# Kernel optimization log

Measured on AMD Instinct MI355X. Metric: run time of the kernel, lower is better.

## Reference

```python
import jax, jax.numpy as jnp
import numpy as np

FEATURE_DIM = 768
NUM_HEADS = 16
HEAD_DIM = FEATURE_DIM // NUM_HEADS
SCALE = HEAD_DIM ** -0.5


def setup_inputs() -> dict:
    key = jax.random.key(0)
    ks = jax.random.split(key, 9)
    B, N, C = 4, 2048, FEATURE_DIM
    s = 0.02
    return {
        "x": jax.random.normal(ks[0], (B, N, C), dtype=jnp.float32),
        "wq": jax.random.normal(ks[1], (C, C), dtype=jnp.float32) * s,
        "bq": jax.random.normal(ks[2], (C,), dtype=jnp.float32) * s,
        "wk": jax.random.normal(ks[3], (C, C), dtype=jnp.float32) * s,
        "bk": jax.random.normal(ks[4], (C,), dtype=jnp.float32) * s,
        "wv": jax.random.normal(ks[5], (C, C), dtype=jnp.float32) * s,
        "bv": jax.random.normal(ks[6], (C,), dtype=jnp.float32) * s,
        "wo": jax.random.normal(ks[7], (C, C), dtype=jnp.float32) * s,
        "bo": jax.random.normal(ks[8], (C,), dtype=jnp.float32) * s,
    }


def reference(x, wq, bq, wk, bk, wv, bv, wo, bo):
    B, N, C = x.shape
    H, D = NUM_HEADS, HEAD_DIM
    # Linear layers use weight of shape (out, in): y = x @ W.T + b
    def proj(w, b):
        return (jnp.einsum("bnc,dc->bnd", x, w) + b).reshape(B, N, H, D).transpose(0, 2, 1, 3)
    q = proj(wq, bq)  # [B,H,N,D]
    k = proj(wk, bk)
    v = proj(wv, bv)
    attn = jnp.einsum("bhnd,bhmd->bhnm", q, k) * SCALE
    attn = jax.nn.softmax(attn, axis=-1)  # dropout = identity (eval mode)
    y = jnp.einsum("bhnm,bhmd->bhnd", attn, v).transpose(0, 2, 1, 3).reshape(B, N, C)
    y = y + x
    out = jnp.einsum("bnc,dc->bnd", y, wo) + bo
    out = out + y
    return out + x
```

## Files before the change

kernel.cpp:

```cpp
#include <hip/hip_runtime.h>
#include <hip/hip_bf16.h>

#define B_ 4
#define N_ 2048
#define C_ 768
#define H_ 16
#define D_ 48
#define SCALE_ 0.14433756729740643f
#define LOG2E_ 1.44269504088896f

using bf16 = __hip_bfloat16;
using bf16x8 = __attribute__((ext_vector_type(8))) short;
using f32x4  = __attribute__((ext_vector_type(4))) float;
using f32x16 = __attribute__((ext_vector_type(16))) float;
using u32x2  = __attribute__((ext_vector_type(2))) unsigned int;
using u32x4  = __attribute__((ext_vector_type(4))) unsigned int;

__device__ __forceinline__ unsigned short f2b(float f) {
  bf16 h = __float2bfloat16(f);
  return *reinterpret_cast<unsigned short*>(&h);
}
__device__ __forceinline__ unsigned int pack2(float lo, float hi) {
  return (unsigned int)f2b(lo) | ((unsigned int)f2b(hi) << 16);
}
__device__ __forceinline__ unsigned int pk2(float lo, float hi) {
  unsigned int r;
  asm("v_cvt_pk_bf16_f32 %0, %1, %2" : "=v"(r) : "v"(lo), "v"(hi));
  return r;
}
__device__ __forceinline__ uint4 ld8f_cvt(const float* p) {
  float4 a = *reinterpret_cast<const float4*>(p);
  float4 b = *reinterpret_cast<const float4*>(p + 4);
  uint4 u;
  u.x = pack2(a.x, a.y); u.y = pack2(a.z, a.w);
  u.z = pack2(b.x, b.y); u.w = pack2(b.z, b.w);
  return u;
}
__device__ __forceinline__ void gload_lds16(const bf16* g, bf16* l) {
  __builtin_amdgcn_global_load_lds(
      (const __attribute__((address_space(1))) unsigned int*)g,
      (__attribute__((address_space(3))) unsigned int*)l, 16, 0, 0);
}

__global__ __launch_bounds__(256) void cvt_bf16(
    const float* __restrict__ x,  const float* __restrict__ wq,
    const float* __restrict__ wk, const float* __restrict__ wv,
    const float* __restrict__ wo,
    bf16* __restrict__ xb, bf16* __restrict__ wqkvb, bf16* __restrict__ wob)
{
  const int job = blockIdx.y;
  const float* src; bf16* dst; int n;
  if (job == 0)      { src = x;  dst = xb;              n = B_ * N_ * C_; }
  else if (job == 1) { src = wq; dst = wqkvb;           n = C_ * C_; }
  else if (job == 2) { src = wk; dst = wqkvb + C_ * C_; n = C_ * C_; }
  else if (job == 3) { src = wv; dst = wqkvb + 2 * C_ * C_; n = C_ * C_; }
  else               { src = wo; dst = wob;             n = C_ * C_; }
  const int stride = gridDim.x * 256 * 8;
  for (int i = (blockIdx.x * 256 + threadIdx.x) * 8; i < n; i += stride)
    *(uint4*)(dst + i) = ld8f_cvt(src + i);
}

__global__ __launch_bounds__(256) void gemm_qkv(
    const bf16* __restrict__ A, const bf16* __restrict__ Bw,
    const float* __restrict__ bq, const float* __restrict__ bk,
    const float* __restrict__ bv,
    bf16* __restrict__ Q, bf16* __restrict__ K, bf16* __restrict__ V)
{
  __shared__ __align__(16) bf16 As[128 * 64];
  __shared__ __align__(16) bf16 Bs[128 * 64];

  const int tid  = threadIdx.x;
  const int lane = tid & 63, wid = tid >> 6;
  const int wm = (wid >> 1) * 64, wn = (wid & 1) * 64;
  const int row0 = blockIdx.y * 128, col0 = blockIdx.x * 128;
  const int mb = lane & 15, g4 = lane >> 4;
  const int srow = lane >> 3;
  const int schunk = (lane & 7) ^ (srow & 7);

  f32x4 acc[4][4];
#pragma unroll
  for (int i = 0; i < 4; ++i)
#pragma unroll
    for (int j = 0; j < 4; ++j) acc[i][j] = (f32x4){0.f, 0.f, 0.f, 0.f};

  for (int k0 = 0; k0 < C_; k0 += 64) {
#pragma unroll
    for (int t = 0; t < 4; ++t) {
      const int rt = wid * 32 + t * 8;
      gload_lds16(A  + (size_t)(row0 + rt + srow) * C_ + k0 + schunk * 8,
                  As + rt * 64);
      gload_lds16(Bw + (size_t)(col0 + rt + srow) * C_ + k0 + schunk * 8,
                  Bs + rt * 64);
    }
    __syncthreads();
#pragma unroll
    for (int ks = 0; ks < 2; ++ks) {
      const int kchunk = ks * 4 + g4;
      bf16x8 af[4], bfr[4];
#pragma unroll
      for (int i = 0; i < 4; ++i) {
        const int row = wm + i * 16 + mb;
        af[i] = *(const bf16x8*)(As + row * 64 + (kchunk ^ (row & 7)) * 8);
      }
#pragma unroll
      for (int j = 0; j < 4; ++j) {
        const int col = wn + j * 16 + mb;
        bfr[j] = *(const bf16x8*)(Bs + col * 64 + (kchunk ^ (col & 7)) * 8);
      }
#pragma unroll
      for (int i = 0; i < 4; ++i)
#pragma unroll
        for (int j = 0; j < 4; ++j)
          acc[i][j] = __builtin_amdgcn_mfma_f32_16x16x32_bf16(af[i], bfr[j], acc[i][j], 0, 0, 0);
    }
    __syncthreads();
  }

  const int z = blockIdx.x / 6;
  const float* bias = (z == 0) ? bq : (z == 1) ? bk : bv;
  bf16* dst = (z == 0) ? Q : (z == 1) ? K : V;
  const float sc = (z == 0) ? (SCALE_ * LOG2E_) : 1.0f;
  const int crow = g4 * 4;
#pragma unroll
  for (int j = 0; j < 4; ++j) {
    const int oo = col0 - z * 768 + wn + j * 16 + mb;
    const int h = oo / D_, d = oo % D_;
    const float bb = bias[oo];
#pragma unroll
    for (int i = 0; i < 4; ++i) {
#pragma unroll
      for (int reg = 0; reg < 4; ++reg) {
        const int r = row0 + wm + i * 16 + crow + reg;
        const int b_ = r >> 11, n = r & (N_ - 1);
        dst[(((size_t)(b_ * H_ + h)) * N_ + n) * D_ + d] =
            __float2bfloat16((acc[i][j][reg] + bb) * sc);
      }
    }
  }
}

__global__ __launch_bounds__(256) void qkv_reshape(
    bf16* __restrict__ Q, bf16* __restrict__ K,
    const bf16* __restrict__ Vtmp, bf16* __restrict__ Vf)
{
  __shared__ short T[64 * 50];
  const int bh = blockIdx.x;
  const int t0 = blockIdx.y * 64;
  const int tid = threadIdx.x;
  const size_t base = (size_t)bh * (N_ * D_) + (size_t)t0 * D_;
#pragma unroll 1
  for (int wbuf = 0; wbuf < 2; ++wbuf) {
    bf16* P = (wbuf ? K : Q) + base;
    for (int cc = tid; cc < 384; cc += 256) {
      const int r = cc / 6, ch = cc % 6;
      bf16x8 v8 = *(const bf16x8*)(P + r * D_ + ch * 8);
#pragma unroll
      for (int e = 0; e < 8; ++e) T[r * 50 + ch * 8 + e] = v8[e];
    }
    __syncthreads();
    for (int w = tid; w < 384; w += 256) {
      const int sub = w / 192, rem = w % 192;
      const int kc = rem / 64, rem2 = rem % 64;
      const int g2 = rem2 >> 5, m5 = rem2 & 31;
      bf16x8 o;
#pragma unroll
      for (int e = 0; e < 8; ++e)
        o[e] = T[(sub * 32 + m5) * 50 + kc * 16 + g2 * 8 + e];
      *(bf16x8*)(P + w * 8) = o;
    }
    __syncthreads();
  }
  {
    const bf16* Pv = Vtmp + base;
    for (int cc = tid; cc < 384; cc += 256) {
      const int r = cc / 6, ch = cc % 6;
      bf16x8 v8 = *(const bf16x8*)(Pv + r * D_ + ch * 8);
#pragma unroll
      for (int e = 0; e < 8; ++e) T[r * 50 + ch * 8 + e] = v8[e];
    }
    __syncthreads();
    bf16* W = Vf + (size_t)bh * (N_ * 64) + (size_t)t0 * 64;
    for (int w = tid; w < 512; w += 256) {
      const int ksl = w >> 7;
      const int dt  = (w >> 6) & 1;
      const int l   = w & 63;
      const int hi = l >> 5, m5 = l & 31;
      bf16x8 o;
      if (dt == 0) {
#pragma unroll
        for (int e = 0; e < 8; ++e)
          o[e] = T[(ksl * 16 + hi * 8 + e) * 50 + m5];
      } else if (m5 < 16) {
#pragma unroll
        for (int e = 0; e < 8; ++e)
          o[e] = T[(ksl * 16 + hi * 8 + e) * 50 + 32 + m5];
      } else {
        const short fill = (m5 == 16) ? (short)0x3F80 : (short)0;
#pragma unroll
        for (int e = 0; e < 8; ++e) o[e] = fill;
      }
      *(bf16x8*)(W + (size_t)(((ksl * 2 + dt) * 64 + l) * 8)) = o;
    }
  }
}

__global__ __launch_bounds__(256, 4) void attn_mfma(
    const bf16* __restrict__ Qf, const bf16* __restrict__ Kf,
    const bf16* __restrict__ Vf, const float* __restrict__ x,
    bf16* __restrict__ Yb)
{
  __shared__ __align__(16) bf16 Ls[2 * 7168];

  const int tid  = threadIdx.x;
  const int lane = tid & 63, wid = tid >> 6;
  const int m5 = lane & 31, hi = lane >> 5;
  const int bh = blockIdx.x;
  const int b_ = bh >> 4, h = bh & 15;
  const int q0 = blockIdx.y * 128 + wid * 32;
  const size_t slab  = (size_t)bh * (N_ * D_);
  const size_t slabV = (size_t)bh * (N_ * 64);

  bf16x8 qf[3];
  const int kgq = q0 >> 5;
#pragma unroll
  for (int kc = 0; kc < 3; ++kc)
    qf[kc] = *(const bf16x8*)(Qf + slab + (size_t)(((kgq * 3 + kc) * 64) + lane) * 8);

  f32x16 zf;
#pragma unroll
  for (int r = 0; r < 16; ++r) zf[r] = 0.f;

  f32x16 Oacc[2];
#pragma unroll
  for (int dt = 0; dt < 2; ++dt)
#pragma unroll
    for (int r = 0; r < 16; ++r) Oacc[dt][r] = 0.f;

  const bf16* kb = Kf + slab  + (size_t)lane * 8;
  const bf16* vb = Vf + slabV + (size_t)lane * 8;
  auto stage = [&](int t, int buf) {
    bf16* dstb = Ls + buf * 7168;
    const bf16* kt = kb + (size_t)t * 3072;
    const bf16* vt = vb + (size_t)t * 4096;
    for (int c = wid; c < 14; c += 4) {
      if (c < 6) gload_lds16(kt + c * 512, dstb + c * 512);
      else       gload_lds16(vt + (c - 6) * 512, dstb + c * 512);
    }
  };

  auto sub = [&](int buf, int s) {
    const bf16* Lb = Ls + buf * 7168 + (size_t)lane * 8;
    bf16x8 kf[3], vA[2][2];
#pragma unroll
    for (int kc = 0; kc < 3; ++kc)
      kf[kc] = *(const bf16x8*)(Lb + (s * 3 + kc) * 512);
#pragma unroll
    for (int ks = 0; ks < 2; ++ks)
#pragma unroll
      for (int dt = 0; dt < 2; ++dt)
        vA[ks][dt] = *(const bf16x8*)(Lb + (6 + s * 4 + ks * 2 + dt) * 512);
    f32x16 S;
    S = __builtin_amdgcn_mfma_f32_32x32x16_bf16(kf[0], qf[0], zf, 0, 0, 0);
    S = __builtin_amdgcn_mfma_f32_32x32x16_bf16(kf[1], qf[1], S, 0, 0, 0);
    S = __builtin_amdgcn_mfma_f32_32x32x16_bf16(kf[2], qf[2], S, 0, 0, 0);
#pragma unroll
    for (int r = 0; r < 16; ++r)
      S[r] = __builtin_amdgcn_exp2f(S[r]);
#pragma unroll
    for (int ks = 0; ks < 2; ++ks) {
      const int qa = ks * 2;
      const unsigned A0 = pk2(S[4 * qa + 0], S[4 * qa + 1]);
      const unsigned A1 = pk2(S[4 * qa + 2], S[4 * qa + 3]);
      const unsigned B0 = pk2(S[4 * qa + 4], S[4 * qa + 5]);
      const unsigned B1 = pk2(S[4 * qa + 6], S[4 * qa + 7]);
      const u32x2 r02 = __builtin_amdgcn_permlane32_swap(A0, B0, false, false);
      const u32x2 r13 = __builtin_amdgcn_permlane32_swap(A1, B1, false, false);
      u32x4 pw;
      pw.x = r02.x; pw.y = r13.x; pw.z = r02.y; pw.w = r13.y;
      const bf16x8 pb = (bf16x8)pw;
      Oacc[0] = __builtin_amdgcn_mfma_f32_32x32x16_bf16(vA[ks][0], pb, Oacc[0], 0, 0, 0);
      Oacc[1] = __builtin_amdgcn_mfma_f32_32x32x16_bf16(vA[ks][1], pb, Oacc[1], 0, 0, 0);
    }
  };

  stage(0, 0);
  __syncthreads();
  int buf = 0;
#pragma unroll 1
  for (int t = 0; t < 32; ++t) {
    if (t + 1 < 32) stage(t + 1, buf ^ 1);
    sub(buf, 0);
    sub(buf, 1);
    __syncthreads();
    buf ^= 1;
  }

  const float lf = Oacc[1][8];
  const unsigned lu = __builtin_bit_cast(unsigned, lf);
  const u32x2 lsw = __builtin_amdgcn_permlane32_swap(lu, lu, false, false);
  const float Lv = __builtin_bit_cast(float, lsw.x);
  const float inv = 1.f / Lv;

  const int n = q0 + m5;
  const size_t rowoff = ((size_t)(b_ * N_ + n)) * C_ + h * D_;
#pragma unroll
  for (int qq = 0; qq < 4; ++qq) {
    const size_t off = rowoff + 8 * qq + 4 * hi;
    const float4 xr = *(const float4*)(x + off);
    u32x2 wv;
    wv.x = pk2(Oacc[0][4 * qq + 0] * inv + xr.x, Oacc[0][4 * qq + 1] * inv + xr.y);
    wv.y = pk2(Oacc[0][4 * qq + 2] * inv + xr.z, Oacc[0][4 * qq + 3] * inv + xr.w);
    *(u32x2*)(Yb + off) = wv;
  }
#pragma unroll
  for (int qq = 0; qq < 2; ++qq) {
    const size_t off = rowoff + 32 + 8 * qq + 4 * hi;
    const float4 xr = *(const float4*)(x + off);
    u32x2 wv;
    wv.x = pk2(Oacc[1][4 * qq + 0] * inv + xr.x, Oacc[1][4 * qq + 1] * inv + xr.y);
    wv.y = pk2(Oacc[1][4 * qq + 2] * inv + xr.z, Oacc[1][4 * qq + 3] * inv + xr.w);
    *(u32x2*)(Yb + off) = wv;
  }
}

__global__ __launch_bounds__(256) void gemm_out(
    const bf16* __restrict__ Yb, const bf16* __restrict__ Bw,
    const float* __restrict__ bo, const float* __restrict__ x,
    float* __restrict__ out)
{
  __shared__ __align__(16) bf16 As[128 * 64];
  __shared__ __align__(16) bf16 Bs[128 * 64];

  const int tid  = threadIdx.x;
  const int lane = tid & 63, wid = tid >> 6;
  const int wm = (wid >> 1) * 64, wn = (wid & 1) * 64;
  const int row0 = blockIdx.y * 128, col0 = blockIdx.x * 128;
  const int mb = lane & 15, g4 = lane >> 4;
  const int srow = lane >> 3;
  const int schunk = (lane & 7) ^ (srow & 7);

  f32x4 acc[4][4];
#pragma unroll
  for (int i = 0; i < 4; ++i)
#pragma unroll
    for (int j = 0; j < 4; ++j) acc[i][j] = (f32x4){0.f, 0.f, 0.f, 0.f};

  for (int k0 = 0; k0 < C_; k0 += 64) {
#pragma unroll
    for (int t = 0; t < 4; ++t) {
      const int rt = wid * 32 + t * 8;
      gload_lds16(Yb + (size_t)(row0 + rt + srow) * C_ + k0 + schunk * 8,
                  As + rt * 64);
      gload_lds16(Bw + (size_t)(col0 + rt + srow) * C_ + k0 + schunk * 8,
                  Bs + rt * 64);
    }
    __syncthreads();
#pragma unroll
    for (int ks = 0; ks < 2; ++ks) {
      const int kchunk = ks * 4 + g4;
      bf16x8 af[4], bfr[4];
#pragma unroll
      for (int i = 0; i < 4; ++i) {
        const int row = wm + i * 16 + mb;
        af[i] = *(const bf16x8*)(As + row * 64 + (kchunk ^ (row & 7)) * 8);
      }
#pragma unroll
      for (int j = 0; j < 4; ++j) {
        const int col = wn + j * 16 + mb;
        bfr[j] = *(const bf16x8*)(Bs + col * 64 + (kchunk ^ (col & 7)) * 8);
      }
#pragma unroll
      for (int i = 0; i < 4; ++i)
#pragma unroll
        for (int j = 0; j < 4; ++j)
          acc[i][j] = __builtin_amdgcn_mfma_f32_16x16x32_bf16(af[i], bfr[j], acc[i][j], 0, 0, 0);
    }
    __syncthreads();
  }

  const int crow = g4 * 4;
#pragma unroll
  for (int j = 0; j < 4; ++j) {
    const int o = col0 + wn + j * 16 + mb;
    const float bb = bo[o];
#pragma unroll
    for (int i = 0; i < 4; ++i) {
#pragma unroll
      for (int reg = 0; reg < 4; ++reg) {
        const int r = row0 + wm + i * 16 + crow + reg;
        const size_t off = (size_t)r * C_ + o;
        out[off] = acc[i][j][reg] + bb + __bfloat162float(Yb[off]) + x[off];
      }
    }
  }
}

extern "C" void kernel_launch(void* const* d_in, const int* in_sizes, int n_in,
                              void* d_out, int out_size, void* d_ws, size_t ws_size,
                              hipStream_t stream)
{
  const float* x  = (const float*)d_in[0];
  const float* wq = (const float*)d_in[1];
  const float* bq = (const float*)d_in[2];
  const float* wk = (const float*)d_in[3];
  const float* bk = (const float*)d_in[4];
  const float* wv = (const float*)d_in[5];
  const float* bv = (const float*)d_in[6];
  const float* wo = (const float*)d_in[7];
  const float* bo = (const float*)d_in[8];
  float* out = (float*)d_out;

  const size_t nEl  = (size_t)B_ * N_ * C_;
  const size_t wEl  = (size_t)C_ * C_;
  const size_t vfEl = (size_t)B_ * H_ * N_ * 64;
  bf16* Q     = (bf16*)d_ws;
  bf16* K     = Q + nEl;
  bf16* Vf    = K + nEl;
  bf16* Yb    = Vf + vfEl;
  bf16* xb    = Yb + nEl;
  bf16* wqkvb = xb + nEl;
  bf16* wob   = wqkvb + 3 * wEl;

  dim3 gcvt(768, 5);
  cvt_bf16<<<gcvt, dim3(256), 0, stream>>>(x, wq, wk, wv, wo, xb, wqkvb, wob);

  dim3 gqkv(18, 64);
  gemm_qkv<<<gqkv, dim3(256), 0, stream>>>(xb, wqkvb, bq, bk, bv, Q, K, Yb);

  dim3 grs(B_ * H_, N_ / 64);
  qkv_reshape<<<grs, dim3(256), 0, stream>>>(Q, K, Yb, Vf);

  dim3 gattn(B_ * H_, N_ / 128);
  attn_mfma<<<gattn, dim3(256), 0, stream>>>(Q, K, Vf, x, Yb);

  dim3 gout(6, 64);
  gemm_out<<<gout, dim3(256), 0, stream>>>(Yb, wob, bo, x, out);
}
```

Baseline: 261.7 us.

## Fuse QKV reshape into GEMM epilogue and triple-buffer attention K/V staging

The QKV GEMM epilogue now writes Q, K and V straight into the MFMA-ready tiled layouts the attention kernel reads, which removes the separate reshape kernel and its extra global round trip. The constant padding columns of the V layout are filled by an extra job in the conversion kernel. Separately, the attention kernel moves to a three-deep LDS ring with only two waves issuing loads, uses explicit vmcnt waits plus a raw barrier in place of syncthreads, and raises wave priority around MFMA bursts. These changes add LDS usage and make correctness depend on the hand-written waitcnt accounting.

Measured after the change: 262.0 us. No clear change (+0.1%).

```diff
diff --git a/kernel.cpp b/kernel.cpp
--- a/kernel.cpp
+++ b/kernel.cpp
@@ -46,9 +46,22 @@
     const float* __restrict__ x,  const float* __restrict__ wq,
     const float* __restrict__ wk, const float* __restrict__ wv,
     const float* __restrict__ wo,
-    bf16* __restrict__ xb, bf16* __restrict__ wqkvb, bf16* __restrict__ wob)
+    bf16* __restrict__ xb, bf16* __restrict__ wqkvb, bf16* __restrict__ wob,
+    bf16* __restrict__ vfp)
 {
   const int job = blockIdx.y;
+  if (job == 5) {
+    for (int u = blockIdx.x * 256 + threadIdx.x; u < 64 * 128 * 32;
+         u += gridDim.x * 256) {
+      const int m5i = u & 15, hb = (u >> 4) & 1, n4 = (u >> 5) & 127,
+                bh = u >> 12;
+      const short fill = (m5i == 0) ? (short)0x3F80 : (short)0;
+      const bf16x8 o = {fill, fill, fill, fill, fill, fill, fill, fill};
+      *(bf16x8*)(vfp + (size_t)bh * 131072 + n4 * 1024 + 512 + hb * 256 +
+                 (16 + m5i) * 8) = o;
+    }
+    return;
+  }
   const float* src; bf16* dst; int n;
   if (job == 0)      { src = x;  dst = xb;              n = B_ * N_ * C_; }
   else if (job == 1) { src = wq; dst = wqkvb;           n = C_ * C_; }
@@ -64,7 +77,7 @@
     const bf16* __restrict__ A, const bf16* __restrict__ Bw,
     const float* __restrict__ bq, const float* __restrict__ bk,
     const float* __restrict__ bv,
-    bf16* __restrict__ Q, bf16* __restrict__ K, bf16* __restrict__ V)
+    bf16* __restrict__ Q, bf16* __restrict__ K, bf16* __restrict__ Vf)
 {
   __shared__ __align__(16) bf16 As[128 * 64];
   __shared__ __align__(16) bf16 Bs[128 * 64];
@@ -117,89 +130,45 @@
   }
 
   const int z = blockIdx.x / 6;
-  const float* bias = (z == 0) ? bq : (z == 1) ? bk : bv;
-  bf16* dst = (z == 0) ? Q : (z == 1) ? K : V;
-  const float sc = (z == 0) ? (SCALE_ * LOG2E_) : 1.0f;
-  const int crow = g4 * 4;
-#pragma unroll
-  for (int j = 0; j < 4; ++j) {
-    const int oo = col0 - z * 768 + wn + j * 16 + mb;
-    const int h = oo / D_, d = oo % D_;
-    const float bb = bias[oo];
-#pragma unroll
-    for (int i = 0; i < 4; ++i) {
-#pragma unroll
-      for (int reg = 0; reg < 4; ++reg) {
-        const int r = row0 + wm + i * 16 + crow + reg;
-        const int b_ = r >> 11, n = r & (N_ - 1);
-        dst[(((size_t)(b_ * H_ + h)) * N_ + n) * D_ + d] =
-            __float2bfloat16((acc[i][j][reg] + bb) * sc);
-      }
-    }
-  }
-}
-
-__global__ __launch_bounds__(256) void qkv_reshape(
-    bf16* __restrict__ Q, bf16* __restrict__ K,
-    const bf16* __restrict__ Vtmp, bf16* __restrict__ Vf)
-{
-  __shared__ short T[64 * 50];
-  const int bh = blockIdx.x;
-  const int t0 = blockIdx.y * 64;
-  const int tid = threadIdx.x;
-  const size_t base = (size_t)bh * (N_ * D_) + (size_t)t0 * D_;
-#pragma unroll 1
-  for (int wbuf = 0; wbuf < 2; ++wbuf) {
-    bf16* P = (wbuf ? K : Q) + base;
-    for (int cc = tid; cc < 384; cc += 256) {
-      const int r = cc / 6, ch = cc % 6;
-      bf16x8 v8 = *(const bf16x8*)(P + r * D_ + ch * 8);
-#pragma unroll
-      for (int e = 0; e < 8; ++e) T[r * 50 + ch * 8 + e] = v8[e];
-    }
-    __syncthreads();
-    for (int w = tid; w < 384; w += 256) {
-      const int sub = w / 192, rem = w % 192;
-      const int kc = rem / 64, rem2 = rem % 64;
-      const int g2 = rem2 >> 5, m5 = rem2 & 31;
-      bf16x8 o;
-#pragma unroll
-      for (int e = 0; e < 8; ++e)
-        o[e] = T[(sub * 32 + m5) * 50 + kc * 16 + g2 * 8 + e];
-      *(bf16x8*)(P + w * 8) = o;
-    }
-    __syncthreads();
-  }
-  {
-    const bf16* Pv = Vtmp + base;
-    for (int cc = tid; cc < 384; cc += 256) {
-      const int r = cc / 6, ch = cc % 6;
-      bf16x8 v8 = *(const bf16x8*)(Pv + r * D_ + ch * 8);
-#pragma unroll
-      for (int e = 0; e < 8; ++e) T[r * 50 + ch * 8 + e] = v8[e];
-    }
-    __syncthreads();
-    bf16* W = Vf + (size_t)bh * (N_ * 64) + (size_t)t0 * 64;
-    for (int w = tid; w < 512; w += 256) {
-      const int ksl = w >> 7;
-      const int dt  = (w >> 6) & 1;
-      const int l   = w & 63;
-      const int hi = l >> 5, m5 = l & 31;
-      bf16x8 o;
-      if (dt == 0) {
-#pragma unroll
-        for (int e = 0; e < 8; ++e)
-          o[e] = T[(ksl * 16 + hi * 8 + e) * 50 + m5];
-      } else if (m5 < 16) {
-#pragma unroll
-        for (int e = 0; e < 8; ++e)
-          o[e] = T[(ksl * 16 + hi * 8 + e) * 50 + 32 + m5];
-      } else {
-        const short fill = (m5 == 16) ? (short)0x3F80 : (short)0;
-#pragma unroll
-        for (int e = 0; e < 8; ++e) o[e] = fill;
-      }
-      *(bf16x8*)(W + (size_t)(((ksl * 2 + dt) * 64 + l) * 8)) = o;
+  const int b_ = row0 >> 11;
+  const int nb = (row0 & (N_ - 1)) + wm;
+  if (z < 2) {
+    const float* bias = (z == 0) ? bq : bk;
+    bf16* dst = (z == 0) ? Q : K;
+    const float sc = (z == 0) ? (SCALE_ * LOG2E_) : 1.0f;
+#pragma unroll
+    for (int j = 0; j < 4; ++j) {
+      const int oo = col0 - z * 768 + wn + j * 16 + mb;
+      const int h = oo / D_, d = oo % D_;
+      const float bb = bias[oo];
+      bf16* slabp = dst + (size_t)(b_ * H_ + h) * (N_ * D_);
+      const int dpart = (d >> 4) * 512 + ((d >> 3) & 1) * 256 + (d & 7);
+#pragma unroll
+      for (int i = 0; i < 4; ++i) {
+        const int base2 = ((nb >> 5) + (i >> 1)) * 1536 + dpart;
+        const int mlo = (i & 1) * 16 + g4 * 4;
+#pragma unroll
+        for (int reg = 0; reg < 4; ++reg)
+          slabp[base2 + (mlo + reg) * 8] =
+              __float2bfloat16((acc[i][j][reg] + bb) * sc);
+      }
+    }
+  } else {
+#pragma unroll
+    for (int j = 0; j < 4; ++j) {
+      const int oo = col0 - 2 * 768 + wn + j * 16 + mb;
+      const int h = oo / D_, d = oo % D_;
+      const float bb = bv[oo];
+      bf16* slabp = Vf + (size_t)(b_ * H_ + h) * (N_ * 64);
+      const int dpart = (d >> 5) * 512 + ((g4 >> 1) * 32 + (d & 31)) * 8 +
+                        (g4 & 1) * 4;
+#pragma unroll
+      for (int i = 0; i < 4; ++i) {
+        u32x2 wv;
+        wv.x = pk2(acc[i][j][0] + bb, acc[i][j][1] + bb);
+        wv.y = pk2(acc[i][j][2] + bb, acc[i][j][3] + bb);
+        *(u32x2*)(slabp + ((nb >> 4) + i) * 1024 + dpart) = wv;
+      }
     }
   }
 }
@@ -209,7 +178,7 @@
     const bf16* __restrict__ Vf, const float* __restrict__ x,
     bf16* __restrict__ Yb)
 {
-  __shared__ __align__(16) bf16 Ls[2 * 7168];
+  __shared__ __align__(16) bf16 Ls[3 * 7168];
 
   const int tid  = threadIdx.x;
   const int lane = tid & 63, wid = tid >> 6;
@@ -239,12 +208,16 @@
   const bf16* kb = Kf + slab  + (size_t)lane * 8;
   const bf16* vb = Vf + slabV + (size_t)lane * 8;
   auto stage = [&](int t, int buf) {
-    bf16* dstb = Ls + buf * 7168;
-    const bf16* kt = kb + (size_t)t * 3072;
-    const bf16* vt = vb + (size_t)t * 4096;
-    for (int c = wid; c < 14; c += 4) {
-      if (c < 6) gload_lds16(kt + c * 512, dstb + c * 512);
-      else       gload_lds16(vt + (c - 6) * 512, dstb + c * 512);
+    if (wid < 2) {
+      bf16* dstb = Ls + buf * 7168;
+      const bf16* kt = kb + (size_t)t * 3072;
+      const bf16* vt = vb + (size_t)t * 4096;
+#pragma unroll
+      for (int cc = 0; cc < 7; ++cc) {
+        const int c = wid * 7 + cc;
+        if (c < 6) gload_lds16(kt + c * 512, dstb + c * 512);
+        else       gload_lds16(vt + (c - 6) * 512, dstb + c * 512);
+      }
     }
   };
 
@@ -260,9 +233,11 @@
       for (int dt = 0; dt < 2; ++dt)
         vA[ks][dt] = *(const bf16x8*)(Lb + (6 + s * 4 + ks * 2 + dt) * 512);
     f32x16 S;
+    __builtin_amdgcn_s_setprio(1);
     S = __builtin_amdgcn_mfma_f32_32x32x16_bf16(kf[0], qf[0], zf, 0, 0, 0);
     S = __builtin_amdgcn_mfma_f32_32x32x16_bf16(kf[1], qf[1], S, 0, 0, 0);
     S = __builtin_amdgcn_mfma_f32_32x32x16_bf16(kf[2], qf[2], S, 0, 0, 0);
+    __builtin_amdgcn_s_setprio(0);
 #pragma unroll
     for (int r = 0; r < 16; ++r)
       S[r] = __builtin_amdgcn_exp2f(S[r]);
@@ -278,21 +253,24 @@
       u32x4 pw;
       pw.x = r02.x; pw.y = r13.x; pw.z = r02.y; pw.w = r13.y;
       const bf16x8 pb = (bf16x8)pw;
+      __builtin_amdgcn_s_setprio(1);
       Oacc[0] = __builtin_amdgcn_mfma_f32_32x32x16_bf16(vA[ks][0], pb, Oacc[0], 0, 0, 0);
       Oacc[1] = __builtin_amdgcn_mfma_f32_32x32x16_bf16(vA[ks][1], pb, Oacc[1], 0, 0, 0);
+      __builtin_amdgcn_s_setprio(0);
     }
   };
 
   stage(0, 0);
-  __syncthreads();
-  int buf = 0;
+  stage(1, 1);
+  asm volatile("s_waitcnt vmcnt(7)" ::: "memory");
 #pragma unroll 1
   for (int t = 0; t < 32; ++t) {
-    if (t + 1 < 32) stage(t + 1, buf ^ 1);
-    sub(buf, 0);
-    sub(buf, 1);
-    __syncthreads();
-    buf ^= 1;
+    __builtin_amdgcn_s_barrier();
+    if (t + 2 < 32) stage(t + 2, (t + 2) % 3);
+    sub(t % 3, 0);
+    sub(t % 3, 1);
+    if (t < 30)       asm volatile("s_waitcnt vmcnt(7)" ::: "memory");
+    else if (t == 30) asm volatile("s_waitcnt vmcnt(0)" ::: "memory");
   }
 
   const float lf = Oacc[1][8];
@@ -421,14 +399,11 @@
   bf16* wqkvb = xb + nEl;
   bf16* wob   = wqkvb + 3 * wEl;
 
-  dim3 gcvt(768, 5);
-  cvt_bf16<<<gcvt, dim3(256), 0, stream>>>(x, wq, wk, wv, wo, xb, wqkvb, wob);
+  dim3 gcvt(768, 6);
+  cvt_bf16<<<gcvt, dim3(256), 0, stream>>>(x, wq, wk, wv, wo, xb, wqkvb, wob, Vf);
 
   dim3 gqkv(18, 64);
-  gemm_qkv<<<gqkv, dim3(256), 0, stream>>>(xb, wqkvb, bq, bk, bv, Q, K, Yb);
-
-  dim3 grs(B_ * H_, N_ / 64);
-  qkv_reshape<<<grs, dim3(256), 0, stream>>>(Q, K, Yb, Vf);
+  gemm_qkv<<<gqkv, dim3(256), 0, stream>>>(xb, wqkvb, bq, bk, bv, Q, K, Vf);
 
   dim3 gattn(B_ * H_, N_ / 128);
   attn_mfma<<<gattn, dim3(256), 0, stream>>>(Q, K, Vf, x, Yb);
```
